# Optimization experiments

Measured on AMD Instinct MI355X. Metric: run time of the kernel, lower is better.

The kernel has to match this reference:

```python
import jax, jax.numpy as jnp
import numpy as np

S = 100          # samples per ray (torch.linspace steps=100)
SIZE = 100.0     # box size per axis -> voxel_range = [-50, 50]


def _trilinear(vol, pts):
    """torch.F.grid_sample(mode='bilinear', align_corners=True, padding='zeros') in 3D.
    vol: [C, D, H, W]; pts: [..., 3] with (x, y, z) in [-1, 1] mapping to (W, H, D).
    Returns [C, ...]."""
    C, D, H, W = vol.shape
    shp = pts.shape[:-1]
    p = pts.reshape(-1, 3)
    ix = (p[:, 0] + 1.0) * 0.5 * (W - 1)
    iy = (p[:, 1] + 1.0) * 0.5 * (H - 1)
    iz = (p[:, 2] + 1.0) * 0.5 * (D - 1)
    x0 = jnp.floor(ix); y0 = jnp.floor(iy); z0 = jnp.floor(iz)
    fx = ix - x0; fy = iy - y0; fz = iz - z0
    x0i = x0.astype(jnp.int32); y0i = y0.astype(jnp.int32); z0i = z0.astype(jnp.int32)
    out = jnp.zeros((C, p.shape[0]), vol.dtype)
    for dz in (0, 1):
        for dy in (0, 1):
            for dx in (0, 1):
                xi = x0i + dx; yi = y0i + dy; zi = z0i + dz
                wgt = ((fx if dx else 1.0 - fx) *
                       (fy if dy else 1.0 - fy) *
                       (fz if dz else 1.0 - fz))
                inb = ((xi >= 0) & (xi < W) & (yi >= 0) & (yi < H) &
                       (zi >= 0) & (zi < D))
                xc = jnp.clip(xi, 0, W - 1)
                yc = jnp.clip(yi, 0, H - 1)
                zc = jnp.clip(zi, 0, D - 1)
                v = vol[:, zc, yc, xc]                      # [C, N]
                out = out + v * (wgt * inb.astype(vol.dtype))[None, :]
    return out.reshape((C,) + shp)


def setup_inputs() -> dict:
    key = jax.random.key(0)
    k1, k2, k3 = jax.random.split(key, 3)
    R = 65536
    # origins strictly inside the box [-50,50]^3
    ray_origins = jax.random.uniform(k1, (R, 3), jnp.float32) * 80.0 - 40.0
    # all-positive unit directions (original intersection code does not swap
    # t_min/t_max, so positive components guarantee valid t0 < t1)
    d = jnp.abs(jax.random.normal(k2, (R, 3), jnp.float32)) + 1e-3
    ray_directions = d / jnp.linalg.norm(d, axis=-1, keepdims=True)
    volume = jax.random.normal(k3, (11, 128, 128, 128), jnp.float32)
    return {"ray_origins": ray_origins, "ray_directions": ray_directions,
            "volume": volume}


def reference(ray_origins, ray_directions, volume):
    lo, hi = -SIZE / 2.0, SIZE / 2.0
    inv = 1.0 / ray_directions                          # [R,3]
    t_min = (lo - ray_origins) * inv
    t_max = (hi - ray_origins) * inv
    t0 = jnp.maximum(jnp.max(t_min, axis=-1), 0.0)      # [R]
    t1 = jnp.min(t_max, axis=-1)                        # [R]
    frac = jnp.linspace(0.0, 1.0, S)                    # [S]
    ts = t0[:, None] + (t1 - t0)[:, None] * frac[None, :]      # [R,S]
    points = ray_origins[:, None, :] + ts[..., None] * ray_directions[:, None, :]
    grid = points / (SIZE / 2.0)                        # (p - lo)/(hi-lo)*2 - 1
    samp = _trilinear(volume, grid)                     # [11, R, S]
    c = samp[:3]            # [3,R,S]
    alpha = samp[3]         # [R,S]
    w = samp[4:7]           # [3,R,S]
    lamb = samp[7]          # [R,S]
    s = samp[8:11]          # [3,R,S]
    trans = jnp.cumprod(1.0 - alpha + 1e-10, axis=-1)   # inclusive cumprod, as original
    wts = alpha * trans                                 # [R,S]
    acc_c = jnp.sum(wts[None] * c, axis=-1)             # [3,R]
    acc_w = jnp.sum(wts[None] * w, axis=-1)             # [3,R]
    acc_lamb = jnp.sum(wts * lamb, axis=-1)             # [R]
    acc_s = jnp.sum(wts[None] * s, axis=-1)             # [3,R]
    dot = jnp.sum(acc_s * ray_directions.T, axis=0)     # [R]
    out = acc_c + acc_w * jnp.exp(acc_lamb * (dot - 1.0))[None]
    return out.T                                        # [R,3]
```

## Files before the change

kernel.cpp:

```cpp
#include <hip/hip_runtime.h>


constexpr int   S_SAMPLES = 100;
constexpr int   GN        = 128;
constexpr int   GV        = GN * GN * GN;
constexpr float HALF_SIZE = 50.0f;

typedef float v2f __attribute__((ext_vector_type(2)));

__global__ __launch_bounds__(256) void vol_pack_kernel(
    const float* __restrict__ vol, uint32_t* __restrict__ vol8) {
  const int v = blockIdx.x * 256 + threadIdx.x;
  if (v >= GV) return;
  float c[12];
#pragma unroll
  for (int i = 0; i < 11; ++i) c[i] = vol[(size_t)i * GV + v];
  c[11] = 0.0f;
  uint4 w;
  {
    int a;
    a = __builtin_amdgcn_cvt_pk_fp8_f32(c[0], c[1], 0, false);
    a = __builtin_amdgcn_cvt_pk_fp8_f32(c[2], c[3], a, true);
    w.x = (uint32_t)a;
    a = __builtin_amdgcn_cvt_pk_fp8_f32(c[4], c[5], 0, false);
    a = __builtin_amdgcn_cvt_pk_fp8_f32(c[6], c[7], a, true);
    w.y = (uint32_t)a;
    a = __builtin_amdgcn_cvt_pk_fp8_f32(c[8], c[9], 0, false);
    a = __builtin_amdgcn_cvt_pk_fp8_f32(c[10], c[11], a, true);
    w.z = (uint32_t)a;
    w.w = 0u;
  }
  reinterpret_cast<uint4*>(vol8)[v] = w;
}

template <bool TR>
__global__ __launch_bounds__(256) void render_kernel(
    const float* __restrict__ ro, const float* __restrict__ rd,
    const float* __restrict__ vol, const uint32_t* __restrict__ vol8,
    float* __restrict__ out, int R) {
  const int lane = threadIdx.x & 63;
  const int ray  = blockIdx.x * 4 + (threadIdx.x >> 6);
  if (ray >= R) return;

  const float ox = ro[ray * 3 + 0], oy = ro[ray * 3 + 1], oz = ro[ray * 3 + 2];
  const float dx = rd[ray * 3 + 0], dy = rd[ray * 3 + 1], dz = rd[ray * 3 + 2];

  const float ivx = 1.0f / dx, ivy = 1.0f / dy, ivz = 1.0f / dz;
  const float tnx = (-HALF_SIZE - ox) * ivx;
  const float tny = (-HALF_SIZE - oy) * ivy;
  const float tnz = (-HALF_SIZE - oz) * ivz;
  const float tpx = ( HALF_SIZE - ox) * ivx;
  const float tpy = ( HALF_SIZE - oy) * ivy;
  const float tpz = ( HALF_SIZE - oz) * ivz;
  const float t0 = fmaxf(fmaxf(tnx, fmaxf(tny, tnz)), 0.0f);
  const float t1 = fminf(tpx, fminf(tpy, tpz));

  float ch[2][11];
#pragma unroll
  for (int b = 0; b < 2; ++b) {
#pragma unroll
    for (int k = 0; k < 11; ++k) ch[b][k] = 0.0f;
    const int s = lane + 64 * b;
    if (s < S_SAMPLES) {
      const float frac = (float)s * (1.0f / 99.0f);
      const float t  = t0 + (t1 - t0) * frac;
      const float px = ox + t * dx, py = oy + t * dy, pz = oz + t * dz;
      const float gx = px / HALF_SIZE, gy = py / HALF_SIZE, gz = pz / HALF_SIZE;
      const float fix = (gx + 1.0f) * 0.5f * 127.0f;
      const float fiy = (gy + 1.0f) * 0.5f * 127.0f;
      const float fiz = (gz + 1.0f) * 0.5f * 127.0f;
      const float x0f = floorf(fix), y0f = floorf(fiy), z0f = floorf(fiz);
      const float fx = fix - x0f, fy = fiy - y0f, fz = fiz - z0f;
      const int x0 = (int)x0f, y0 = (int)y0f, z0 = (int)z0f;
      const float wx[2] = {1.0f - fx, fx};
      const float wy[2] = {1.0f - fy, fy};
      const float wz[2] = {1.0f - fz, fz};
#pragma unroll
      for (int cz = 0; cz < 2; ++cz) {
#pragma unroll
        for (int cy = 0; cy < 2; ++cy) {
#pragma unroll
          for (int cx = 0; cx < 2; ++cx) {
            const int xi = x0 + cx, yi = y0 + cy, zi = z0 + cz;
            const bool inb = ((unsigned)xi < 128u) && ((unsigned)yi < 128u) &&
                             ((unsigned)zi < 128u);
            const float w =
                wx[cx] * wy[cy] * wz[cz] * (inb ? 1.0f : 0.0f);
            const int xc = min(max(xi, 0), 127);
            const int yc = min(max(yi, 0), 127);
            const int zc = min(max(zi, 0), 127);
            const int vidx = (zc * GN + yc) * GN + xc;
            if (TR) {
              const uint4 wd =
                  reinterpret_cast<const uint4*>(vol8)[vidx];
              const v2f c01 = __builtin_amdgcn_cvt_pk_f32_fp8(wd.x, false);
              const v2f c23 = __builtin_amdgcn_cvt_pk_f32_fp8(wd.x, true);
              const v2f c45 = __builtin_amdgcn_cvt_pk_f32_fp8(wd.y, false);
              const v2f c67 = __builtin_amdgcn_cvt_pk_f32_fp8(wd.y, true);
              const v2f c89 = __builtin_amdgcn_cvt_pk_f32_fp8(wd.z, false);
              const v2f cab = __builtin_amdgcn_cvt_pk_f32_fp8(wd.z, true);
              ch[b][0]  += w * c01[0];  ch[b][1]  += w * c01[1];
              ch[b][2]  += w * c23[0];  ch[b][3]  += w * c23[1];
              ch[b][4]  += w * c45[0];  ch[b][5]  += w * c45[1];
              ch[b][6]  += w * c67[0];  ch[b][7]  += w * c67[1];
              ch[b][8]  += w * c89[0];  ch[b][9]  += w * c89[1];
              ch[b][10] += w * cab[0];
            } else {
#pragma unroll
              for (int c = 0; c < 11; ++c)
                ch[b][c] += w * vol[c * GV + vidx];
            }
          }
        }
      }
    }
  }

  const float alpha0 = ch[0][3];
  const float alpha1 = ch[1][3];

  const float v0 = 1.0f - alpha0 + 1e-10f;
  const float v1 = (lane + 64 < S_SAMPLES) ? (1.0f - alpha1 + 1e-10f) : 1.0f;

  float p = v0;
#pragma unroll
  for (int off = 1; off < 64; off <<= 1) {
    const float u = __shfl_up(p, (unsigned)off, 64);
    if (lane >= off) p *= u;
  }
  const float tr0    = p;
  const float total0 = __shfl(p, 63, 64);

  p = v1;
#pragma unroll
  for (int off = 1; off < 64; off <<= 1) {
    const float u = __shfl_up(p, (unsigned)off, 64);
    if (lane >= off) p *= u;
  }
  const float tr1 = p * total0;

  const float w0 = alpha0 * tr0;
  const float w1 = alpha1 * tr1;

  float q[10];
  {
    const int map[10] = {0, 1, 2, 4, 5, 6, 7, 8, 9, 10};
#pragma unroll
    for (int i = 0; i < 10; ++i)
      q[i] = w0 * ch[0][map[i]] + w1 * ch[1][map[i]];
  }
#pragma unroll
  for (int off = 32; off >= 1; off >>= 1) {
#pragma unroll
    for (int i = 0; i < 10; ++i) q[i] += __shfl_xor(q[i], off, 64);
  }

  if (lane < 3) {
    const float dot = q[7] * dx + q[8] * dy + q[9] * dz;
    const float e   = expf(q[6] * (dot - 1.0f));
    float r = q[lane] + q[3 + lane] * e;
    r = fminf(fmaxf(r, -3.0e38f), 3.0e38f);
    out[ray * 3 + lane] = r;
  }
}

extern "C" void kernel_launch(void* const* d_in, const int* in_sizes, int n_in,
                              void* d_out, int out_size, void* d_ws,
                              size_t ws_size, hipStream_t stream) {
  const float* ro  = (const float*)d_in[0];
  const float* rd  = (const float*)d_in[1];
  const float* vol = (const float*)d_in[2];
  float* out = (float*)d_out;
  const int R = in_sizes[0] / 3;

  const size_t need = (size_t)GV * 16;
  const int render_blocks = (R + 3) / 4;

  if (ws_size >= need) {
    uint32_t* vol8 = (uint32_t*)d_ws;
    vol_pack_kernel<<<GV / 256, 256, 0, stream>>>(vol, vol8);
    render_kernel<true><<<render_blocks, 256, 0, stream>>>(
        ro, rd, vol, vol8, out, R);
  } else {
    render_kernel<false><<<render_blocks, 256, 0, stream>>>(
        ro, rd, vol, nullptr, out, R);
  }
}
```

Baseline: 280.2 us.

## Sort rays by Morton-coded origin cell and swizzle blocks across XCDs

Adds a counting sort of rays, keyed by a 4-bit-per-axis Morton code of the ray origin, built from four small kernels (zero histogram, key+histogram, scan, scatter). Rendering goes through the sorted index so nearby rays run together, and block IDs are remapped so consecutive sorted chunks land on the same XCD. The goal is better L2 reuse of the fp8-packed volume gathers. The volume pack kernel is also vectorised to float4 loads. This adds four extra launches, atomics and one level of indirection for ray loads.

```diff
diff --git a/kernel.cpp b/kernel.cpp
--- a/kernel.cpp
+++ b/kernel.cpp
@@ -5,42 +5,120 @@
 constexpr int   GN        = 128;
 constexpr int   GV        = GN * GN * GN;
 constexpr float HALF_SIZE = 50.0f;
+constexpr int   NB        = 4096;
 
 typedef float v2f __attribute__((ext_vector_type(2)));
+
+__device__ __forceinline__ float f4el(const float4& f, int k) {
+  switch (k) { case 0: return f.x; case 1: return f.y; case 2: return f.z;
+               default: return f.w; }
+}
 
 __global__ __launch_bounds__(256) void vol_pack_kernel(
     const float* __restrict__ vol, uint32_t* __restrict__ vol8) {
-  const int v = blockIdx.x * 256 + threadIdx.x;
-  if (v >= GV) return;
-  float c[12];
-#pragma unroll
-  for (int i = 0; i < 11; ++i) c[i] = vol[(size_t)i * GV + v];
-  c[11] = 0.0f;
-  uint4 w;
-  {
-    int a;
-    a = __builtin_amdgcn_cvt_pk_fp8_f32(c[0], c[1], 0, false);
-    a = __builtin_amdgcn_cvt_pk_fp8_f32(c[2], c[3], a, true);
+  const int t = blockIdx.x * 256 + threadIdx.x;
+  if (t >= GV / 4) return;
+  const float4* v4 = reinterpret_cast<const float4*>(vol);
+  float4 c[11];
+#pragma unroll
+  for (int i = 0; i < 11; ++i) c[i] = v4[(size_t)i * (GV / 4) + t];
+  uint4* o8 = reinterpret_cast<uint4*>(vol8);
+#pragma unroll
+  for (int k = 0; k < 4; ++k) {
+    uint4 w; int a;
+    a = __builtin_amdgcn_cvt_pk_fp8_f32(f4el(c[0], k), f4el(c[1], k), 0, false);
+    a = __builtin_amdgcn_cvt_pk_fp8_f32(f4el(c[2], k), f4el(c[3], k), a, true);
     w.x = (uint32_t)a;
-    a = __builtin_amdgcn_cvt_pk_fp8_f32(c[4], c[5], 0, false);
-    a = __builtin_amdgcn_cvt_pk_fp8_f32(c[6], c[7], a, true);
+    a = __builtin_amdgcn_cvt_pk_fp8_f32(f4el(c[4], k), f4el(c[5], k), 0, false);
+    a = __builtin_amdgcn_cvt_pk_fp8_f32(f4el(c[6], k), f4el(c[7], k), a, true);
     w.y = (uint32_t)a;
-    a = __builtin_amdgcn_cvt_pk_fp8_f32(c[8], c[9], 0, false);
-    a = __builtin_amdgcn_cvt_pk_fp8_f32(c[10], c[11], a, true);
+    a = __builtin_amdgcn_cvt_pk_fp8_f32(f4el(c[8], k), f4el(c[9], k), 0, false);
+    a = __builtin_amdgcn_cvt_pk_fp8_f32(f4el(c[10], k), 0.0f,          a, true);
     w.z = (uint32_t)a;
     w.w = 0u;
-  }
-  reinterpret_cast<uint4*>(vol8)[v] = w;
+    o8[(size_t)t * 4 + k] = w;
+  }
+}
+
+__global__ __launch_bounds__(256) void zero_hist_kernel(uint32_t* __restrict__ h) {
+  const int i = blockIdx.x * 256 + threadIdx.x;
+  if (i < NB) h[i] = 0u;
+}
+
+__device__ __forceinline__ uint32_t spread4(uint32_t a) {
+  return (a & 1u) | ((a & 2u) << 2) | ((a & 4u) << 4) | ((a & 8u) << 6);
+}
+
+__global__ __launch_bounds__(256) void ray_key_hist_kernel(
+    const float* __restrict__ ro, uint32_t* __restrict__ keys,
+    uint32_t* __restrict__ hist, int R) {
+  const int r = blockIdx.x * 256 + threadIdx.x;
+  if (r >= R) return;
+  const float x = ro[r * 3 + 0], y = ro[r * 3 + 1], z = ro[r * 3 + 2];
+  const int cx = min(max((int)((x + 40.0f) * 0.2f), 0), 15);
+  const int cy = min(max((int)((y + 40.0f) * 0.2f), 0), 15);
+  const int cz = min(max((int)((z + 40.0f) * 0.2f), 0), 15);
+  const uint32_t key = spread4((uint32_t)cx) | (spread4((uint32_t)cy) << 1) |
+                       (spread4((uint32_t)cz) << 2);
+  keys[r] = key;
+  atomicAdd(&hist[key], 1u);
+}
+
+__global__ __launch_bounds__(1024) void scan_kernel(
+    const uint32_t* __restrict__ hist, uint32_t* __restrict__ cursor) {
+  const int t = threadIdx.x;
+  const int lane = t & 63, wid = t >> 6;
+  __shared__ uint32_t wtot[16];
+  const uint32_t v0 = hist[t * 4 + 0], v1 = hist[t * 4 + 1];
+  const uint32_t v2 = hist[t * 4 + 2], v3 = hist[t * 4 + 3];
+  const uint32_t tsum = v0 + v1 + v2 + v3;
+  uint32_t ws = tsum;
+#pragma unroll
+  for (int off = 1; off < 64; off <<= 1) {
+    const uint32_t u = __shfl_up(ws, (unsigned)off, 64);
+    if (lane >= off) ws += u;
+  }
+  if (lane == 63) wtot[wid] = ws;
+  __syncthreads();
+  if (t < 16) {
+    uint32_t w = wtot[t];
+#pragma unroll
+    for (int off = 1; off < 16; off <<= 1) {
+      const uint32_t u = __shfl_up(w, (unsigned)off, 16);
+      if (t >= off) w += u;
+    }
+    wtot[t] = w;
+  }
+  __syncthreads();
+  const uint32_t wbase = wid ? wtot[wid - 1] : 0u;
+  uint32_t run = wbase + (ws - tsum);
+  cursor[t * 4 + 0] = run; run += v0;
+  cursor[t * 4 + 1] = run; run += v1;
+  cursor[t * 4 + 2] = run; run += v2;
+  cursor[t * 4 + 3] = run;
+}
+
+__global__ __launch_bounds__(256) void ray_scatter_kernel(
+    const uint32_t* __restrict__ keys, uint32_t* __restrict__ cursor,
+    uint32_t* __restrict__ sorted, int R) {
+  const int r = blockIdx.x * 256 + threadIdx.x;
+  if (r >= R) return;
+  const uint32_t pos = atomicAdd(&cursor[keys[r]], 1u);
+  sorted[pos] = (uint32_t)r;
 }
 
 template <bool TR>
 __global__ __launch_bounds__(256) void render_kernel(
     const float* __restrict__ ro, const float* __restrict__ rd,
     const float* __restrict__ vol, const uint32_t* __restrict__ vol8,
-    float* __restrict__ out, int R) {
+    const uint32_t* __restrict__ sorted, float* __restrict__ out, int R) {
   const int lane = threadIdx.x & 63;
-  const int ray  = blockIdx.x * 4 + (threadIdx.x >> 6);
-  if (ray >= R) return;
+  const int nb  = (int)gridDim.x;
+  const int bid = (int)blockIdx.x;
+  const int sb  = ((nb & 7) == 0) ? ((bid & 7) * (nb >> 3) + (bid >> 3)) : bid;
+  const int gid = sb * 4 + ((int)threadIdx.x >> 6);
+  if (gid >= R) return;
+  const int ray = sorted ? (int)sorted[gid] : gid;
 
   const float ox = ro[ray * 3 + 0], oy = ro[ray * 3 + 1], oz = ro[ray * 3 + 2];
   const float dx = rd[ray * 3 + 0], dy = rd[ray * 3 + 1], dz = rd[ray * 3 + 2];
@@ -91,8 +169,7 @@
             const int zc = min(max(zi, 0), 127);
             const int vidx = (zc * GN + yc) * GN + xc;
             if (TR) {
-              const uint4 wd =
-                  reinterpret_cast<const uint4*>(vol8)[vidx];
+              const uint4 wd = reinterpret_cast<const uint4*>(vol8)[vidx];
               const v2f c01 = __builtin_amdgcn_cvt_pk_f32_fp8(wd.x, false);
               const v2f c23 = __builtin_amdgcn_cvt_pk_f32_fp8(wd.x, true);
               const v2f c45 = __builtin_amdgcn_cvt_pk_f32_fp8(wd.y, false);
@@ -173,16 +250,39 @@
   float* out = (float*)d_out;
   const int R = in_sizes[0] / 3;
 
-  const size_t need = (size_t)GV * 16;
+  const size_t vol8_b   = (size_t)GV * 16;
+  const size_t keys_b   = (size_t)R * 4;
+  const size_t hist_b   = (size_t)NB * 4;
+  const size_t off_keys   = vol8_b;
+  const size_t off_hist   = off_keys + keys_b;
+  const size_t off_cursor = off_hist + hist_b;
+  const size_t off_sorted = off_cursor + hist_b;
+  const size_t need_full  = off_sorted + keys_b;
+
   const int render_blocks = (R + 3) / 4;
-
-  if (ws_size >= need) {
+  const int rblocks256    = (R + 255) / 256;
+
+  if (ws_size >= need_full) {
+    char* ws = (char*)d_ws;
+    uint32_t* vol8   = (uint32_t*)ws;
+    uint32_t* keys   = (uint32_t*)(ws + off_keys);
+    uint32_t* hist   = (uint32_t*)(ws + off_hist);
+    uint32_t* cursor = (uint32_t*)(ws + off_cursor);
+    uint32_t* sorted = (uint32_t*)(ws + off_sorted);
+    vol_pack_kernel<<<(GV / 4 + 255) / 256, 256, 0, stream>>>(vol, vol8);
+    zero_hist_kernel<<<(NB + 255) / 256, 256, 0, stream>>>(hist);
+    ray_key_hist_kernel<<<rblocks256, 256, 0, stream>>>(ro, keys, hist, R);
+    scan_kernel<<<1, 1024, 0, stream>>>(hist, cursor);
+    ray_scatter_kernel<<<rblocks256, 256, 0, stream>>>(keys, cursor, sorted, R);
+    render_kernel<true><<<render_blocks, 256, 0, stream>>>(
+        ro, rd, vol, vol8, sorted, out, R);
+  } else if (ws_size >= vol8_b) {
     uint32_t* vol8 = (uint32_t*)d_ws;
-    vol_pack_kernel<<<GV / 256, 256, 0, stream>>>(vol, vol8);
+    vol_pack_kernel<<<(GV / 4 + 255) / 256, 256, 0, stream>>>(vol, vol8);
     render_kernel<true><<<render_blocks, 256, 0, stream>>>(
-        ro, rd, vol, vol8, out, R);
+        ro, rd, vol, vol8, nullptr, out, R);
   } else {
     render_kernel<false><<<render_blocks, 256, 0, stream>>>(
-        ro, rd, vol, nullptr, out, R);
-  }
-}
+        ro, rd, vol, nullptr, nullptr, out, R);
+  }
+}
```

New measurement: 315.0 us. +12.4%, slower.
